# Kernel optimization log

Measured on AMD Instinct MI355X. Metric: run time of the kernel, lower is better.

The kernel has to match this reference:

```python
import jax, jax.numpy as jnp
import numpy as np
from jax.scipy.special import logsumexp

BS, SEQ, DM = 4, 4096, 1024
H, HD = 16, 64
BLK = 128
NB = SEQ // BLK          # 32 blocks
MAX_NB = 32
N_ITERS = 5
TEMP = 1.0
CLIP = 1.0


def setup_inputs() -> dict:
    key = jax.random.key(0)
    ks = jax.random.split(key, 12)
    s = 0.02
    return {
        'inputs_q': jax.random.normal(ks[0], (BS, SEQ, DM), jnp.float32),
        'wq': jax.random.normal(ks[1], (DM, H, HD), jnp.float32) * s,
        'bq': jnp.zeros((H, HD), jnp.float32),
        'wk': jax.random.normal(ks[2], (DM, H, HD), jnp.float32) * s,
        'bk': jnp.zeros((H, HD), jnp.float32),
        'wv': jax.random.normal(ks[3], (DM, H, HD), jnp.float32) * s,
        'bv': jnp.zeros((H, HD), jnp.float32),
        'w_sort': jax.random.normal(ks[4], (H, HD, MAX_NB), jnp.float32) * s,
        'b_sort': jnp.zeros((MAX_NB,), jnp.float32),
        'wo': jax.random.normal(ks[5], (H, HD, DM), jnp.float32) * s,
        'bo': jnp.zeros((DM,), jnp.float32),
    }


def sinkhorn_operator(log_alpha, n_iters=N_ITERS, temp=TEMP, clip=CLIP):
    # non-causal path of the original: iterative row/col log-normalization
    n = log_alpha.shape[1]
    la = jnp.reshape(log_alpha, (-1, n, n)) / temp
    for _ in range(n_iters):
        la = la - logsumexp(la, axis=2, keepdims=True)  # row normalize
        la = la - logsumexp(la, axis=1, keepdims=True)  # col normalize
    return jnp.exp(jnp.clip(la, -clip, clip))


def reference(inputs_q, wq, bq, wk, bk, wv, bv, w_sort, b_sort, wo, bo):
    bs, qlen, _ = inputs_q.shape
    nb = qlen // BLK
    # QKV projections: (bs, seq, H, HD)
    q = jnp.einsum('bsf,fhd->bshd', inputs_q, wq) + bq
    k = jnp.einsum('bsf,fhd->bshd', inputs_q, wk) + bk  # self-attention: inputs_kv = inputs_q
    v = jnp.einsum('bsf,fhd->bshd', inputs_q, wv) + bv
    # block reshape: (bs, nb, BLK, H, HD)
    qb = q.reshape(bs, nb, BLK, H, HD)
    kb = k.reshape(bs, nb, BLK, H, HD)
    vb = v.reshape(bs, nb, BLK, H, HD)
    # sort network: pool keys within block, project (H,HD)->MAX_NB
    sum_key = jnp.sum(kb, axis=2)                                   # (bs, nb, H, HD)
    sort_out = jnp.einsum('bnhd,hdm->bnm', sum_key, w_sort) + b_sort
    sort_mat = sort_out[:, :, :nb]                                  # (bs, nb, nb)
    perm = sinkhorn_operator(sort_mat)                              # (bs, nb, nb)
    # soft block sorting of keys/values
    sorted_k = jnp.einsum('bnm,bmshd->bnshd', perm, kb)
    sorted_v = jnp.einsum('bnm,bmshd->bnshd', perm, vb)
    # attend within each block to [local kv ; sorted kv]
    kcat = jnp.concatenate([kb, sorted_k], axis=2)                  # (bs, nb, 2BLK, H, HD)
    vcat = jnp.concatenate([vb, sorted_v], axis=2)
    scale = 1.0 / jnp.sqrt(jnp.float32(HD))
    logits = jnp.einsum('bnqhd,bnkhd->bnhqk', qb * scale, kcat)     # (bs, nb, H, BLK, 2BLK)
    w = jax.nn.softmax(logits, axis=-1)
    x = jnp.einsum('bnhqk,bnkhd->bnqhd', w, vcat)                   # (bs, nb, BLK, H, HD)
    x = x.reshape(bs, qlen, H, HD)
    return jnp.einsum('bshd,hdf->bsf', x, wo) + bo
```

## Files before the change

kernel.cpp:

```cpp
#include <hip/hip_runtime.h>
#include <stdint.h>

typedef short bf16x8 __attribute__((ext_vector_type(8)));
typedef float f32x4 __attribute__((ext_vector_type(4)));
typedef unsigned short u16;
typedef unsigned short u16x4 __attribute__((ext_vector_type(4)));

#define AS1 __attribute__((address_space(1)))
#define AS3 __attribute__((address_space(3)))

__device__ __forceinline__ void gll16(const void* g, void* l) {
  __builtin_amdgcn_global_load_lds((const AS1 uint32_t*)g, (AS3 uint32_t*)l, 16, 0, 0);
}

__device__ __forceinline__ f32x4 mfma16(bf16x8 a, bf16x8 b, f32x4 c) {
  return __builtin_amdgcn_mfma_f32_16x16x32_bf16(a, b, c, 0, 0, 0);
}

__device__ __forceinline__ u16 f2bf(float f) {
  union { float f; uint32_t u; } c; c.f = f;
  uint32_t r = c.u + 0x7FFFu + ((c.u >> 16) & 1u);
  return (u16)(r >> 16);
}
__device__ __forceinline__ float bf2f(u16 h) {
  union { uint32_t u; float f; } c; c.u = ((uint32_t)h) << 16; return c.f;
}

__global__ __launch_bounds__(256) void k_cast(const float* __restrict__ in, u16* __restrict__ out) {
  int i = (blockIdx.x * 256 + threadIdx.x) * 4;
  float4 v = *(const float4*)(in + i);
  u16x4 r; r.x = f2bf(v.x); r.y = f2bf(v.y); r.z = f2bf(v.z); r.w = f2bf(v.w);
  *(u16x4*)(out + i) = r;
}

__global__ __launch_bounds__(1024) void k_transpose4(
    const float* __restrict__ wq, const float* __restrict__ wk,
    const float* __restrict__ wv, const float* __restrict__ wo,
    u16* __restrict__ Wqkvt, u16* __restrict__ Wot) {
  __shared__ float t[32][33];
  const float* src; u16* dst;
  int z = blockIdx.z;
  if (z == 0)      { src = wq; dst = Wqkvt; }
  else if (z == 1) { src = wk; dst = Wqkvt + 1024 * 1024; }
  else if (z == 2) { src = wv; dst = Wqkvt + 2 * 1024 * 1024; }
  else             { src = wo; dst = Wot; }
  int tx = threadIdx.x, ty = threadIdx.y;
  t[ty][tx] = src[(size_t)(blockIdx.y * 32 + ty) * 1024 + blockIdx.x * 32 + tx];
  __syncthreads();
  dst[(size_t)(blockIdx.x * 32 + ty) * 1024 + blockIdx.y * 32 + tx] = f2bf(t[tx][ty]);
}

__device__ __forceinline__ void gemm256_loop(
    const u16* __restrict__ Ag, const u16* __restrict__ Bg,
    u16* lds, int m0, int n0, f32x4 (&acc)[8][4])
{
  const int tid = threadIdx.x, lane = tid & 63, w = tid >> 6;
  const int wm = w >> 2, wn = w & 3;
  const int l8 = lane >> 3, c7 = lane & 7;
  const int mm = lane & 15, quad = lane >> 4;
  const int ch0 = (quad ^ (mm & 7)) * 8;
  const int ch1 = ((quad ^ (mm & 7)) ^ 4) * 8;

  const u16* aSt = Ag + (size_t)(m0 + w * 8 + l8) * 1024 + (c7 ^ l8) * 8;
  const u16* bSt = Bg + (size_t)(n0 + w * 8 + l8) * 1024 + (c7 ^ l8) * 8;
  u16* ldsAw = lds + w * 512;
  u16* ldsBw = lds + 32768 + w * 512;
  const u16* aR0 = lds + (wm * 128 + mm) * 64 + ch0;
  const u16* aR1 = lds + (wm * 128 + mm) * 64 + ch1;
  const u16* bR0 = lds + 32768 + (wn * 64 + mm) * 64 + ch0;
  const u16* bR1 = lds + 32768 + (wn * 64 + mm) * 64 + ch1;

#define STA(q, kt, buf) gll16(aSt + (q) * 65536 + (kt) * 64, ldsAw + (buf) * 16384 + (q) * 4096)
#define STB(q, kt, buf) gll16(bSt + (q) * 65536 + (kt) * 64, ldsBw + (buf) * 16384 + (q) * 4096)

#define LDA(C, MH) do {                                                                  \
    _Pragma("unroll")                                                                    \
    for (int i = 0; i < 4; ++i) {                                                        \
      af[i][0] = *(const bf16x8*)(aR0 + (C) * 16384 + ((MH) * 64 + i * 16) * 64);        \
      af[i][1] = *(const bf16x8*)(aR1 + (C) * 16384 + ((MH) * 64 + i * 16) * 64);        \
    }                                                                                    \
  } while (0)
#define LDB(C, NH) do {                                                                  \
    _Pragma("unroll")                                                                    \
    for (int j = 0; j < 2; ++j) {                                                        \
      bf[j][0] = *(const bf16x8*)(bR0 + (C) * 16384 + ((NH) * 32 + j * 16) * 64);        \
      bf[j][1] = *(const bf16x8*)(bR1 + (C) * 16384 + ((NH) * 32 + j * 16) * 64);        \
    }                                                                                    \
  } while (0)
#define MMQ(MH, NH) do {                                                                 \
    __builtin_amdgcn_s_barrier();                                                        \
    asm volatile("s_waitcnt lgkmcnt(0)" ::: "memory");                                   \
    __builtin_amdgcn_sched_barrier(0);                                                   \
    __builtin_amdgcn_s_setprio(1);                                                       \
    _Pragma("unroll")                                                                    \
    for (int ks = 0; ks < 2; ++ks)                                                       \
      _Pragma("unroll")                                                                  \
      for (int i = 0; i < 4; ++i)                                                        \
        _Pragma("unroll")                                                                \
        for (int j = 0; j < 2; ++j)                                                      \
          acc[(MH) * 4 + i][(NH) * 2 + j] =                                              \
              mfma16(af[i][ks], bf[j][ks], acc[(MH) * 4 + i][(NH) * 2 + j]);             \
    __builtin_amdgcn_s_setprio(0);                                                       \
  } while (0)

#define TILE(TT, C) do {                                                                 \
    const int t1 = (TT) + 1, t2 = (TT) + 2;                                              \
    const bool sB = t1 < 16, sA = t2 < 16;                                               \
    LDA(C, 0); LDB(C, 0); if (sB) { STB(0, t1, 1 - (C)); STB(1, t1, 1 - (C)); }          \
    MMQ(0, 0);                                                                           \
    __builtin_amdgcn_s_barrier();                                                        \
    LDB(C, 1); if (sB) { STB(2, t1, 1 - (C)); STB(3, t1, 1 - (C)); }                     \
    if (sA) { STA(0, t2, C); STA(2, t2, C); }                                            \
    MMQ(0, 1);                                                                           \
    __builtin_amdgcn_s_barrier();                                                        \
    LDA(C, 1);                                                                           \
    MMQ(1, 1);                                                                           \
    __builtin_amdgcn_s_barrier();                                                        \
    LDB(C, 0); if (sA) { STA(1, t2, C); STA(3, t2, C); }                                 \
    MMQ(1, 0);                                                                           \
    if ((TT) < 14)       asm volatile("s_waitcnt vmcnt(4)" ::: "memory");                \
    else if ((TT) == 14) asm volatile("s_waitcnt vmcnt(0)" ::: "memory");                \
    __builtin_amdgcn_s_barrier();                                                        \
  } while (0)

#pragma unroll
  for (int i = 0; i < 8; ++i)
#pragma unroll
    for (int j = 0; j < 4; ++j) acc[i][j] = (f32x4){0.f, 0.f, 0.f, 0.f};

  STA(0, 0, 0); STA(1, 0, 0); STA(2, 0, 0); STA(3, 0, 0);
  STB(0, 0, 0); STB(1, 0, 0); STB(2, 0, 0); STB(3, 0, 0);
  STA(0, 1, 1); STA(1, 1, 1); STA(2, 1, 1); STA(3, 1, 1);
  asm volatile("s_waitcnt vmcnt(4)" ::: "memory");
  __builtin_amdgcn_s_barrier();

#pragma unroll 1
  for (int t = 0; t < 16; t += 2) {
    bf16x8 af[4][2]; bf16x8 bf[2][2];
    TILE(t, 0);
    TILE(t + 1, 1);
  }
#undef TILE
#undef MMQ
#undef LDA
#undef LDB
#undef STA
#undef STB
}

__global__ __launch_bounds__(512, 2) void k_gemm_qkv(
    const u16* __restrict__ A, const u16* __restrict__ Bt,
    const float* __restrict__ bq, const float* __restrict__ bk, const float* __restrict__ bv,
    u16* __restrict__ Qb, u16* __restrict__ Kb, u16* __restrict__ Vbt, float* __restrict__ sumk)
{
  __shared__ __align__(16) u16 LDS[65536];
  int lin = blockIdx.x + 12 * blockIdx.y;
  int nb = (lin & 7) * 96 + (lin >> 3);
  const int m0 = (nb / 12) * 256, n0 = (nb % 12) * 256;
  f32x4 acc[8][4];
  gemm256_loop(A, Bt, LDS, m0, n0, acc);

  const int tid = threadIdx.x, lane = tid & 63, w = tid >> 6;
  const int wm = w >> 2, wn = w & 3;
  const int mm = lane & 15, quad = lane >> 4;
  const int sel = n0 >> 10;
  const float* bias = sel == 0 ? bq : (sel == 1 ? bk : bv);

  if (sel == 2) {
    u16* W = LDS + w * 8192;
#pragma unroll
    for (int nf = 0; nf < 4; ++nf) {
      int d = nf * 16 + mm;
      float bval = bias[((n0 & 1023) + wn * 64 + nf * 16 + mm)];
#pragma unroll
      for (int mf = 0; mf < 8; ++mf) {
        int c = mf * 4 + quad;
        u16x4 pk;
        pk.x = f2bf(acc[mf][nf][0] + bval);
        pk.y = f2bf(acc[mf][nf][1] + bval);
        pk.z = f2bf(acc[mf][nf][2] + bval);
        pk.w = f2bf(acc[mf][nf][3] + bval);
        *(u16x4*)(W + d * 128 + (c ^ (d & 15)) * 4) = pk;
      }
    }
    asm volatile("s_waitcnt lgkmcnt(0)" ::: "memory");
    int h_w = ((n0 & 1023) >> 6) + wn;
    int b_ = m0 >> 12;
    int c = lane & 31, dpar = lane >> 5;
    size_t gbase = ((size_t)(b_ * 16 + h_w) * 64) * 4096 + (m0 & 4095) + wm * 128 + c * 4;
#pragma unroll
    for (int dd = 0; dd < 32; ++dd) {
      int d = dd * 2 + dpar;
      u16x4 v = *(const u16x4*)(W + d * 128 + (c ^ (d & 15)) * 4);
      *(u16x4*)(Vbt + gbase + (size_t)d * 4096) = v;
    }
    return;
  }

  const float scl = sel == 0 ? 0.125f : 1.0f;
#pragma unroll
  for (int nf = 0; nf < 4; ++nf) {
    int ngl = n0 + wn * 64 + nf * 16 + mm;
    int nq = ngl & 1023;
    int h = nq >> 6, d = nq & 63;
    float bval = bias[nq];
#pragma unroll
    for (int mf = 0; mf < 8; ++mf)
#pragma unroll
      for (int r = 0; r < 4; ++r) {
        int mg = m0 + wm * 128 + mf * 16 + quad * 4 + r;
        int b_ = mg >> 12, s = mg & 4095;
        float v = (acc[mf][nf][r] + bval) * scl;
        if (sel == 0) Qb[((size_t)(b_ * 16 + h) * 4096 + s) * 64 + d] = f2bf(v);
        else          Kb[((size_t)(b_ * 16 + h) * 4096 + s) * 64 + d] = f2bf(v);
      }
  }

  if (sel == 1) {
#pragma unroll
    for (int nf = 0; nf < 4; ++nf) {
      float ssum = 0.f;
#pragma unroll
      for (int mf = 0; mf < 8; ++mf)
#pragma unroll
        for (int r = 0; r < 4; ++r) ssum += acc[mf][nf][r];
      ssum += __shfl_xor(ssum, 16);
      ssum += __shfl_xor(ssum, 32);
      if (quad == 0) {
        int colg = (n0 - 1024) + wn * 64 + nf * 16 + mm;
        int b_ = m0 >> 12, nb2 = ((m0 >> 7) & 31) + wm;
        sumk[(size_t)(b_ * 32 + nb2) * 1024 + colg] = ssum + 128.f * bias[colg];
      }
    }
  }
}

__global__ __launch_bounds__(512, 2) void k_gemm_out(
    const u16* __restrict__ A, const u16* __restrict__ Bt,
    const float* __restrict__ bo, float* __restrict__ out)
{
  __shared__ __align__(16) u16 LDS[65536];
  int lin = blockIdx.x + 4 * blockIdx.y;
  int nb = (lin & 7) * 32 + (lin >> 3);
  const int m0 = (nb / 4) * 256, n0 = (nb % 4) * 256;
  f32x4 acc[8][4];
  gemm256_loop(A, Bt, LDS, m0, n0, acc);

  const int tid = threadIdx.x, lane = tid & 63, w = tid >> 6;
  const int wm = w >> 2, wn = w & 3;
  const int mm = lane & 15, quad = lane >> 4;
#pragma unroll
  for (int nf = 0; nf < 4; ++nf) {
    int ng = n0 + wn * 64 + nf * 16 + mm;
    float bval = bo[ng];
#pragma unroll
    for (int mf = 0; mf < 8; ++mf)
#pragma unroll
      for (int r = 0; r < 4; ++r) {
        int mg = m0 + wm * 128 + mf * 16 + quad * 4 + r;
        out[(size_t)mg * 1024 + ng] = acc[mf][nf][r] + bval;
      }
  }
}

__global__ __launch_bounds__(256) void k_sortmm(const float* __restrict__ sumk, const float* __restrict__ wsort,
                                                const float* __restrict__ bsort, float* __restrict__ so) {
  __shared__ float red[256];
  int n = blockIdx.x, b = blockIdx.y, t = threadIdx.x;
  int m = t & 31, kp = t >> 5;
  const float* row = sumk + (size_t)(b * 32 + n) * 1024;
  float acc = 0.f;
  for (int c = kp * 128; c < kp * 128 + 128; ++c) acc += row[c] * wsort[c * 32 + m];
  red[t] = acc;
  __syncthreads();
  if (t < 32) {
    float s = bsort[t];
#pragma unroll
    for (int q = 0; q < 8; ++q) s += red[q * 32 + t];
    so[(size_t)(b * 32 + n) * 32 + t] = s;
  }
}

__global__ __launch_bounds__(32) void k_sinkhorn(const float* __restrict__ so, float* __restrict__ perm) {
  __shared__ float A[32][33];
  int b = blockIdx.x, t = threadIdx.x;
  for (int i = 0; i < 32; ++i) A[i][t] = so[(size_t)(b * 32 + i) * 32 + t];
  __syncthreads();
  for (int it = 0; it < 5; ++it) {
    {
      float mx = -1e30f;
      for (int j = 0; j < 32; ++j) mx = fmaxf(mx, A[t][j]);
      float s = 0.f;
      for (int j = 0; j < 32; ++j) s += __expf(A[t][j] - mx);
      float l = mx + __logf(s);
      for (int j = 0; j < 32; ++j) A[t][j] -= l;
    }
    __syncthreads();
    {
      float mx = -1e30f;
      for (int j = 0; j < 32; ++j) mx = fmaxf(mx, A[j][t]);
      float s = 0.f;
      for (int j = 0; j < 32; ++j) s += __expf(A[j][t] - mx);
      float l = mx + __logf(s);
      for (int j = 0; j < 32; ++j) A[j][t] -= l;
    }
    __syncthreads();
  }
  for (int i = 0; i < 32; ++i)
    perm[(size_t)(b * 32 + i) * 32 + t] = __expf(fminf(fmaxf(A[i][t], -1.f), 1.f));
}

__global__ __launch_bounds__(256) void k_mix(
    const u16* __restrict__ Kb, const u16* __restrict__ Vbt, const float* __restrict__ perm,
    u16* __restrict__ Ksort, u16* __restrict__ Vsort)
{
  __shared__ float P[32][32];
  int b = blockIdx.z, y = blockIdx.y, xg = blockIdx.x;
  int tid = threadIdx.x;
#pragma unroll
  for (int i = 0; i < 4; ++i) {
    int idx = i * 256 + tid;
    P[idx >> 5][idx & 31] = perm[b * 1024 + idx];
  }
  __syncthreads();
  if (y < 16) {
    int h = y;
    int ss = xg * 4 + (tid >> 6), d = tid & 63;
    const u16* Kg = Kb + (size_t)(b * 16 + h) * 262144;
    float xk[32];
#pragma unroll
    for (int m = 0; m < 32; ++m) xk[m] = bf2f(Kg[(size_t)(m * 128 + ss) * 64 + d]);
    size_t tbase = (size_t)((b * 16 + h) * 32) * 8192;
#pragma unroll
    for (int nn = 0; nn < 32; ++nn) {
      float sk = 0.f;
#pragma unroll
      for (int m4 = 0; m4 < 8; ++m4) {
        float4 pv = *(const float4*)&P[nn][m4 * 4];
        sk += pv.x * xk[m4 * 4 + 0] + pv.y * xk[m4 * 4 + 1] + pv.z * xk[m4 * 4 + 2] + pv.w * xk[m4 * 4 + 3];
      }
      Ksort[tbase + (size_t)nn * 8192 + ss * 64 + d] = f2bf(sk);
    }
  } else {
    int h = y - 16;
    int d = xg * 2 + (tid >> 7), ss = tid & 127;
    const u16* Vg = Vbt + ((size_t)(b * 16 + h) * 64 + d) * 4096;
    float xv[32];
#pragma unroll
    for (int m = 0; m < 32; ++m) xv[m] = bf2f(Vg[m * 128 + ss]);
    size_t tbase = (size_t)((b * 16 + h) * 32) * 8192;
#pragma unroll
    for (int nn = 0; nn < 32; ++nn) {
      float sv = 0.f;
#pragma unroll
      for (int m4 = 0; m4 < 8; ++m4) {
        float4 pv = *(const float4*)&P[nn][m4 * 4];
        sv += pv.x * xv[m4 * 4 + 0] + pv.y * xv[m4 * 4 + 1] + pv.z * xv[m4 * 4 + 2] + pv.w * xv[m4 * 4 + 3];
      }
      Vsort[tbase + (size_t)nn * 8192 + d * 128 + ss] = f2bf(sv);
    }
  }
}

__global__ __launch_bounds__(256, 2) void k_attn(
    const u16* __restrict__ Qb, const u16* __restrict__ Kb, const u16* __restrict__ Ksort,
    const u16* __restrict__ Vbt, const u16* __restrict__ Vsort, u16* __restrict__ X)
{
  __shared__ u16 Ks[16384];
  __shared__ u16 Vlo[8192];
  __shared__ u16 Vhi[8192];
  int tid = threadIdx.x, lane = tid & 63, w = tid >> 6;
  int n = blockIdx.x, h = blockIdx.y, b = blockIdx.z;
  size_t bh = (size_t)(b * 16 + h);
  size_t tileK = bh * 32 + n;

  {
    int l8 = lane >> 3, sl8 = lane & 7;
    const u16* Korig = Kb + (bh * 4096 + (size_t)n * 128) * 64;
    const u16* Ksrt  = Ksort + tileK * 8192;
#pragma unroll
    for (int c = 0; c < 8; ++c) {
      int cc = w * 8 + c;
      int r = cc * 8 + l8;
      int pk = sl8 ^ (r & 7);
      const u16* src = (cc < 16) ? (Korig + (size_t)r * 64 + pk * 8)
                                 : (Ksrt + (size_t)(r - 128) * 64 + pk * 8);
      gll16(src, Ks + cc * 512);
    }
    int l16 = lane >> 4, sl16 = lane & 15;
    const u16* Vorig = Vbt + bh * 262144 + (size_t)n * 128;
    const u16* Vsrt  = Vsort + tileK * 8192;
#pragma unroll
    for (int c = 0; c < 4; ++c) {
      int cc = w * 4 + c;
      int d = cc * 4 + l16;
      int pv = sl16 ^ (d & 15);
      gll16(Vorig + (size_t)d * 4096 + pv * 8, Vlo + cc * 512);
      gll16(Vsrt + (size_t)d * 128 + pv * 8, Vhi + cc * 512);
    }
  }

  int mm = lane & 15, quad = lane >> 4;
  bf16x8 qf[2][2];
  {
    size_t qrow = bh * 4096 + n * 128 + w * 32;
#pragma unroll
    for (int mt = 0; mt < 2; ++mt)
#pragma unroll
      for (int ks = 0; ks < 2; ++ks)
        qf[mt][ks] = *(const bf16x8*)(Qb + (qrow + mt * 16 + mm) * 64 + ks * 32 + quad * 8);
  }
  __syncthreads();

  f32x4 S[2][16];
#pragma unroll
  for (int mt = 0; mt < 2; ++mt)
#pragma unroll
    for (int nt = 0; nt < 16; ++nt) S[mt][nt] = (f32x4){0.f, 0.f, 0.f, 0.f};
#pragma unroll
  for (int nt = 0; nt < 16; ++nt) {
    int kk = nt * 16 + mm;
#pragma unroll
    for (int ks = 0; ks < 2; ++ks) {
      int ch = (ks * 4 + quad) ^ (kk & 7);
      bf16x8 bk = *(const bf16x8*)(Ks + kk * 64 + ch * 8);
      S[0][nt] = mfma16(qf[0][ks], bk, S[0][nt]);
      S[1][nt] = mfma16(qf[1][ks], bk, S[1][nt]);
    }
  }

  float mx[2][4], ls[2][4];
#pragma unroll
  for (int mt = 0; mt < 2; ++mt)
#pragma unroll
    for (int r = 0; r < 4; ++r) {
      float v = S[mt][0][r];
#pragma unroll
      for (int nt = 1; nt < 16; ++nt) v = fmaxf(v, S[mt][nt][r]);
#pragma unroll
      for (int o = 1; o < 16; o <<= 1) v = fmaxf(v, __shfl_xor(v, o));
      mx[mt][r] = v;
    }
#pragma unroll
  for (int mt = 0; mt < 2; ++mt)
#pragma unroll
    for (int nt = 0; nt < 16; ++nt)
#pragma unroll
      for (int r = 0; r < 4; ++r)
        S[mt][nt][r] = __expf(S[mt][nt][r] - mx[mt][r]);
#pragma unroll
  for (int mt = 0; mt < 2; ++mt)
#pragma unroll
    for (int r = 0; r < 4; ++r) {
      float s = 0.f;
#pragma unroll
      for (int nt = 0; nt < 16; ++nt) s += S[mt][nt][r];
#pragma unroll
      for (int o = 1; o < 16; o <<= 1) s += __shfl_xor(s, o);
      ls[mt][r] = s;
    }

  __syncthreads();

  u16* Pw = Ks + w * 4096;
  f32x4 O[2][4];
#pragma unroll
  for (int mt = 0; mt < 2; ++mt)
#pragma unroll
    for (int dt = 0; dt < 4; ++dt) O[mt][dt] = (f32x4){0.f, 0.f, 0.f, 0.f};

#pragma unroll
  for (int half = 0; half < 2; ++half) {
    const u16* Vp = half == 0 ? Vlo : Vhi;
#pragma unroll
    for (int mt = 0; mt < 2; ++mt)
#pragma unroll
      for (int nt8 = 0; nt8 < 8; ++nt8) {
        int nt = half * 8 + nt8;
        int kkl = nt8 * 16 + mm;
#pragma unroll
        for (int r = 0; r < 4; ++r) {
          int q = mt * 16 + quad * 4 + r;
          int ch = (kkl >> 3) ^ (q & 15);
          Pw[q * 128 + ch * 8 + (kkl & 7)] = f2bf(S[mt][nt][r]);
        }
      }
#pragma unroll
    for (int ksl = 0; ksl < 4; ++ksl) {
      bf16x8 pa[2];
#pragma unroll
      for (int mt = 0; mt < 2; ++mt) {
        int q = mt * 16 + mm;
        int ch = (ksl * 4 + quad) ^ (q & 15);
        pa[mt] = *(const bf16x8*)(Pw + q * 128 + ch * 8);
      }
#pragma unroll
      for (int dt = 0; dt < 4; ++dt) {
        int d = dt * 16 + mm;
        int ch = (ksl * 4 + quad) ^ (d & 15);
        bf16x8 vb = *(const bf16x8*)(Vp + d * 128 + ch * 8);
        O[0][dt] = mfma16(pa[0], vb, O[0][dt]);
        O[1][dt] = mfma16(pa[1], vb, O[1][dt]);
      }
    }
  }

#pragma unroll
  for (int mt = 0; mt < 2; ++mt)
#pragma unroll
    for (int dt = 0; dt < 4; ++dt)
#pragma unroll
      for (int r = 0; r < 4; ++r) {
        int q = w * 32 + mt * 16 + quad * 4 + r;
        float val = O[mt][dt][r] / ls[mt][r];
        size_t row = (size_t)b * 4096 + n * 128 + q;
        X[row * 1024 + h * 64 + dt * 16 + mm] = f2bf(val);
      }
}

extern "C" void kernel_launch(void* const* d_in, const int* in_sizes, int n_in,
                              void* d_out, int out_size, void* d_ws, size_t ws_size,
                              hipStream_t stream) {
  const float* inq   = (const float*)d_in[0];
  const float* wq    = (const float*)d_in[1];
  const float* bq    = (const float*)d_in[2];
  const float* wk    = (const float*)d_in[3];
  const float* bk    = (const float*)d_in[4];
  const float* wv    = (const float*)d_in[5];
  const float* bv    = (const float*)d_in[6];
  const float* wsort = (const float*)d_in[7];
  const float* bsort = (const float*)d_in[8];
  const float* wo    = (const float*)d_in[9];
  const float* bo    = (const float*)d_in[10];
  float* out = (float*)d_out;

  char* ws = (char*)d_ws;
  size_t off = 0;
  auto alloc = [&](size_t bytes) { char* p = ws + off; off += (bytes + 255) & ~(size_t)255; return p; };
  u16*  Qb    = (u16*)alloc(33554432);
  u16*  Kb    = (u16*)alloc(33554432);
  u16*  Vbt   = (u16*)alloc(33554432);
  u16*  Ksort = (u16*)alloc(33554432);
  u16*  Vsort = (u16*)alloc(33554432);
  u16*  Abf   = (u16*)alloc(33554432);
  u16*  Wqkvt = (u16*)alloc(6291456);
  u16*  Wot   = (u16*)alloc(2097152);
  float* sumk = (float*)alloc(524288);
  float* so   = (float*)alloc(16384);
  float* perm = (float*)alloc(16384);
  u16*  X = Abf;

  k_cast<<<16384, 256, 0, stream>>>(inq, Abf);
  k_transpose4<<<dim3(32, 32, 4), dim3(32, 32), 0, stream>>>(wq, wk, wv, wo, Wqkvt, Wot);
  k_gemm_qkv<<<dim3(12, 64), 512, 0, stream>>>(Abf, Wqkvt, bq, bk, bv, Qb, Kb, Vbt, sumk);
  k_sortmm<<<dim3(32, 4), 256, 0, stream>>>(sumk, wsort, bsort, so);
  k_sinkhorn<<<4, 32, 0, stream>>>(so, perm);
  k_mix<<<dim3(32, 32, 4), 256, 0, stream>>>(Kb, Vbt, perm, Ksort, Vsort);
  k_attn<<<dim3(32, 16, 4), 256, 0, stream>>>(Qb, Kb, Ksort, Vbt, Vsort, X);
  k_gemm_out<<<dim3(4, 64), 512, 0, stream>>>(X, Wot, bo, out);
}
```

Baseline: 446.9 us.

## Double-buffer B fragments in GEMM main loop and stage Q/K stores through LDS

The GEMM inner tile now loads B fragments into two register sets (bfA/bfB). This lets the next B fragment load overlap the current MFMA group, and it removes several per-subtile barriers and lgkmcnt waits. The Q/K epilogue now writes bf16 results into per-wave LDS scratch and then copies them to global memory as 16-byte vector stores, replacing the scattered 2-byte stores. This uses more registers, which could affect occupancy at 2 blocks per CU. Dropping barriers also risks LDS hazards if the remaining synchronization is not sufficient.

```diff
diff --git a/kernel.cpp b/kernel.cpp
--- a/kernel.cpp
+++ b/kernel.cpp
@@ -80,17 +80,14 @@
       af[i][1] = *(const bf16x8*)(aR1 + (C) * 16384 + ((MH) * 64 + i * 16) * 64);        \
     }                                                                                    \
   } while (0)
-#define LDB(C, NH) do {                                                                  \
+#define LDBv(C, NH, DST) do {                                                            \
     _Pragma("unroll")                                                                    \
     for (int j = 0; j < 2; ++j) {                                                        \
-      bf[j][0] = *(const bf16x8*)(bR0 + (C) * 16384 + ((NH) * 32 + j * 16) * 64);        \
-      bf[j][1] = *(const bf16x8*)(bR1 + (C) * 16384 + ((NH) * 32 + j * 16) * 64);        \
+      DST[j][0] = *(const bf16x8*)(bR0 + (C) * 16384 + ((NH) * 32 + j * 16) * 64);       \
+      DST[j][1] = *(const bf16x8*)(bR1 + (C) * 16384 + ((NH) * 32 + j * 16) * 64);       \
     }                                                                                    \
   } while (0)
-#define MMQ(MH, NH) do {                                                                 \
-    __builtin_amdgcn_s_barrier();                                                        \
-    asm volatile("s_waitcnt lgkmcnt(0)" ::: "memory");                                   \
-    __builtin_amdgcn_sched_barrier(0);                                                   \
+#define MM(MH, NH, BF) do {                                                              \
     __builtin_amdgcn_s_setprio(1);                                                       \
     _Pragma("unroll")                                                                    \
     for (int ks = 0; ks < 2; ++ks)                                                       \
@@ -99,28 +96,41 @@
         _Pragma("unroll")                                                                \
         for (int j = 0; j < 2; ++j)                                                      \
           acc[(MH) * 4 + i][(NH) * 2 + j] =                                              \
-              mfma16(af[i][ks], bf[j][ks], acc[(MH) * 4 + i][(NH) * 2 + j]);             \
+              mfma16(af[i][ks], BF[j][ks], acc[(MH) * 4 + i][(NH) * 2 + j]);             \
     __builtin_amdgcn_s_setprio(0);                                                       \
+  } while (0)
+#define LGKM0 do {                                                                       \
+    asm volatile("s_waitcnt lgkmcnt(0)" ::: "memory");                                   \
+    __builtin_amdgcn_sched_barrier(0);                                                   \
   } while (0)
 
 #define TILE(TT, C) do {                                                                 \
     const int t1 = (TT) + 1, t2 = (TT) + 2;                                              \
     const bool sB = t1 < 16, sA = t2 < 16;                                               \
-    LDA(C, 0); LDB(C, 0); if (sB) { STB(0, t1, 1 - (C)); STB(1, t1, 1 - (C)); }          \
-    MMQ(0, 0);                                                                           \
-    __builtin_amdgcn_s_barrier();                                                        \
-    LDB(C, 1); if (sB) { STB(2, t1, 1 - (C)); STB(3, t1, 1 - (C)); }                     \
+                                                                                \
+    LDA(C, 0); LDBv(C, 0, bfA);                                                          \
+    if (sB) { STB(0, t1, 1 - (C)); STB(1, t1, 1 - (C)); }                                \
+    LGKM0;                                                                               \
+    LDBv(C, 1, bfB);                                                                     \
+    __builtin_amdgcn_sched_barrier(0);                                                   \
+    MM(0, 0, bfA);                                                                       \
+    __builtin_amdgcn_s_barrier();                                                \
+                                                                                \
+    if (sB) { STB(2, t1, 1 - (C)); STB(3, t1, 1 - (C)); }                                \
     if (sA) { STA(0, t2, C); STA(2, t2, C); }                                            \
-    MMQ(0, 1);                                                                           \
-    __builtin_amdgcn_s_barrier();                                                        \
+    LGKM0;                                                                               \
+    MM(0, 1, bfB);                                                                       \
+                                                                   \
     LDA(C, 1);                                                                           \
-    MMQ(1, 1);                                                                           \
-    __builtin_amdgcn_s_barrier();                                                        \
-    LDB(C, 0); if (sA) { STA(1, t2, C); STA(3, t2, C); }                                 \
-    MMQ(1, 0);                                                                           \
+    LGKM0;                                                                               \
+    MM(1, 1, bfB);                                                                       \
+    __builtin_amdgcn_s_barrier();                                                \
+                                                                                \
+    if (sA) { STA(1, t2, C); STA(3, t2, C); }                                            \
+    MM(1, 0, bfA);                                                                       \
     if ((TT) < 14)       asm volatile("s_waitcnt vmcnt(4)" ::: "memory");                \
     else if ((TT) == 14) asm volatile("s_waitcnt vmcnt(0)" ::: "memory");                \
-    __builtin_amdgcn_s_barrier();                                                        \
+    __builtin_amdgcn_s_barrier();                                                \
   } while (0)
 
 #pragma unroll
@@ -136,14 +146,15 @@
 
 #pragma unroll 1
   for (int t = 0; t < 16; t += 2) {
-    bf16x8 af[4][2]; bf16x8 bf[2][2];
+    bf16x8 af[4][2]; bf16x8 bfA[2][2]; bf16x8 bfB[2][2];
     TILE(t, 0);
     TILE(t + 1, 1);
   }
 #undef TILE
-#undef MMQ
+#undef LGKM0
+#undef MM
 #undef LDA
-#undef LDB
+#undef LDBv
 #undef STA
 #undef STB
 }
@@ -165,9 +176,9 @@
   const int mm = lane & 15, quad = lane >> 4;
   const int sel = n0 >> 10;
   const float* bias = sel == 0 ? bq : (sel == 1 ? bk : bv);
+  u16* W = LDS + w * 8192;
 
   if (sel == 2) {
-    u16* W = LDS + w * 8192;
 #pragma unroll
     for (int nf = 0; nf < 4; ++nf) {
       int d = nf * 16 + mm;
@@ -200,20 +211,25 @@
   const float scl = sel == 0 ? 0.125f : 1.0f;
 #pragma unroll
   for (int nf = 0; nf < 4; ++nf) {
-    int ngl = n0 + wn * 64 + nf * 16 + mm;
-    int nq = ngl & 1023;
-    int h = nq >> 6, d = nq & 63;
-    float bval = bias[nq];
+    float bval = bias[(n0 & 1023) + wn * 64 + nf * 16 + mm];
 #pragma unroll
     for (int mf = 0; mf < 8; ++mf)
 #pragma unroll
-      for (int r = 0; r < 4; ++r) {
-        int mg = m0 + wm * 128 + mf * 16 + quad * 4 + r;
-        int b_ = mg >> 12, s = mg & 4095;
-        float v = (acc[mf][nf][r] + bval) * scl;
-        if (sel == 0) Qb[((size_t)(b_ * 16 + h) * 4096 + s) * 64 + d] = f2bf(v);
-        else          Kb[((size_t)(b_ * 16 + h) * 4096 + s) * 64 + d] = f2bf(v);
-      }
+      for (int r = 0; r < 4; ++r)
+        W[(mf * 16 + quad * 4 + r) * 64 + nf * 16 + mm] = f2bf((acc[mf][nf][r] + bval) * scl);
+  }
+  asm volatile("s_waitcnt lgkmcnt(0)" ::: "memory");
+  {
+    int h = ((n0 & 1023) >> 6) + wn;
+    int mg0 = m0 + wm * 128;
+    int b_ = mg0 >> 12;
+    u16* dst = (sel == 0 ? Qb : Kb) + ((size_t)(b_ * 16 + h) * 4096 + (mg0 & 4095)) * 64;
+    int l8 = lane >> 3, c8 = lane & 7;
+#pragma unroll
+    for (int i = 0; i < 16; ++i) {
+      int s = i * 8 + l8;
+      *(bf16x8*)(dst + s * 64 + c8 * 8) = *(const bf16x8*)(W + s * 64 + c8 * 8);
+    }
   }
 
   if (sel == 1) {
```

Result: no change. 438.3 us (-1.9%).
